# Kernel tuning notes

Hardware: AMD Instinct MI355X
Metric: run time of the kernel (lower is better)

The kernel has to match this reference:

```python
import jax, jax.numpy as jnp
import numpy as np

N = 100000
E = 3200000
IN_DIM = 3
HID = 256
OUT_DIM = 3


def setup_inputs() -> dict:
    key = jax.random.key(0)
    ks = jax.random.split(key, 12)
    x = jax.random.normal(ks[0], (N, IN_DIM), dtype=jnp.float32)
    edge_index = jax.random.randint(ks[1], (2, E), 0, N, dtype=jnp.int64)
    def lin(k, fi, fo):
        k1, k2 = jax.random.split(k)
        bound = 1.0 / np.sqrt(fi)
        W = jax.random.uniform(k1, (fi, fo), jnp.float32, -bound, bound)
        b = jax.random.uniform(k2, (fo,), jnp.float32, -bound, bound)
        return W, b
    W0, b0 = lin(ks[2], IN_DIM, HID)
    W1, b1 = lin(ks[3], HID, HID)
    W2, b2 = lin(ks[4], HID, HID)
    W3, b3 = lin(ks[5], HID, OUT_DIM)
    Wr, br = lin(ks[6], IN_DIM, OUT_DIM)
    return {"x": x, "edge_index": edge_index,
            "W0": W0, "b0": b0, "W1": W1, "b1": b1,
            "W2": W2, "b2": b2, "W3": W3, "b3": b3,
            "Wr": Wr, "br": br}


def reference(x, edge_index, W0, b0, W1, b1, W2, b2, W3, b3, Wr, br):
    n = x.shape[0]
    # add self loops, mirroring build_adjacency_matrix
    loops = jnp.arange(n, dtype=edge_index.dtype)
    row = jnp.concatenate([edge_index[0], loops])
    col = jnp.concatenate([edge_index[1], loops])
    # degree of row endpoints, D^{-1/2}[row] * D^{-1/2}[col] edge weights
    deg = jax.ops.segment_sum(jnp.ones_like(row, dtype=x.dtype), row, num_segments=n)
    dinv = jnp.where(deg > 0, jax.lax.rsqrt(deg), 0.0)
    norm = dinv[row] * dinv[col]  # [E+N]

    def propagate(h):
        # A_hat @ h : gather source features, scale, scatter-add to rows
        return jax.ops.segment_sum(norm[:, None] * h[col], row, num_segments=n)

    h = jax.nn.relu(propagate(x) @ W0 + b0)
    h = jax.nn.relu(propagate(h) @ W1 + b1)
    h = jax.nn.relu(propagate(h) @ W2 + b2)
    h = propagate(h) @ W3 + b3  # last layer: no relu
    return h + (x @ Wr + br)
```

## Files before the change

kernel.cpp:

```cpp
#include <hip/hip_runtime.h>
#include <stdint.h>

typedef unsigned short u16;
typedef unsigned int u32;
typedef __attribute__((ext_vector_type(8))) short short8;
typedef __attribute__((ext_vector_type(4))) float f32x4;

#define CAP 6144
#define TILE 4096

__device__ __forceinline__ float b2f_bits(u32 bits){ union{u32 u; float f;} v; v.u=bits; return v.f; }
__device__ __forceinline__ float bf_lo(u32 w){ return b2f_bits(w<<16); }
__device__ __forceinline__ float bf_hi(u32 w){ return b2f_bits(w & 0xffff0000u); }
__device__ __forceinline__ u16 f2bf(float f){
  union{float f; u32 u;} v; v.f=f;
  return (u16)((v.u + 0x7fffu + ((v.u>>16)&1u))>>16);
}

__global__ void zero_k(int* __restrict__ p, int n){
  int i = blockIdx.x*256 + threadIdx.x;
  if(i<n) p[i]=0;
}

__global__ void detect_k(const long long* __restrict__ ei, int* __restrict__ flag, int n, int E){
  __shared__ int sh[256];
  int t = threadIdx.x;
  int lim = E/2 < 2048 ? E/2 : 2048;
  int bad = 0;
  for(int e=t; e<lim; e+=256){
    unsigned long long v = (unsigned long long)ei[e];
    if(v >= (unsigned long long)n) bad = 1;
  }
  sh[t]=bad; __syncthreads();
  for(int off=128; off>0; off>>=1){ if(t<off) sh[t] |= sh[t+off]; __syncthreads(); }
  if(t==0) *flag = sh[0];
}

__device__ __forceinline__ int edge_at(const void* eiv, int is32, long long idx){
  return is32 ? ((const int*)eiv)[idx] : (int)((const long long*)eiv)[idx];
}
__device__ __forceinline__ int clampi(int v, int lo, int hi){
  return v < lo ? lo : (v > hi ? hi : v);
}

__global__ __launch_bounds__(256) void binA_k(const void* __restrict__ eiv, const int* __restrict__ flag,
                        int* __restrict__ gcur, u32* __restrict__ gbuf, int E, int n, int nbuck){
  __shared__ int hist[1024];
  __shared__ int base[1024];
  __shared__ int cur[1024];
  __shared__ int wsum[256];
  __shared__ u32 stage[TILE];
  int t = threadIdx.x;
  long long e0 = (long long)blockIdx.x * TILE;
  int cnt = (int)((long long)E - e0 < TILE ? (long long)E - e0 : TILE);
  int is32 = *flag;
  for(int i=t; i<nbuck; i+=256){ hist[i]=0; cur[i]=0; }
  __syncthreads();
  int eb[16]; u32 ep[16]; int ec=0;
  #pragma unroll
  for(int k=0;k<16;k++){
    int i = t + k*256;
    if(i<cnt){
      long long e = e0 + i;
      int r = clampi(edge_at(eiv,is32,e),0,n-1);
      int c = clampi(edge_at(eiv,is32,(long long)E+e),0,n-1);
      eb[ec] = r>>7;
      ep[ec] = ((u32)(r&127)<<17) | (u32)c;
      atomicAdd(&hist[eb[ec]],1);
      ec++;
    }
  }
  __syncthreads();
  int l[4]; int tot=0;
  #pragma unroll
  for(int j=0;j<4;j++){ int idx=t*4+j; l[j]=(idx<nbuck)?hist[idx]:0; tot+=l[j]; }
  wsum[t]=tot; __syncthreads();
  for(int off=1;off<256;off<<=1){
    int x = (t>=off)?wsum[t-off]:0;
    __syncthreads();
    wsum[t]+=x;
    __syncthreads();
  }
  int excl = wsum[t]-tot;
  #pragma unroll
  for(int j=0;j<4;j++){ int idx=t*4+j; if(idx<nbuck) base[idx]=excl; excl+=l[j]; }
  __syncthreads();
  for(int k=0;k<ec;k++){
    int b = eb[k];
    int slot = base[b] + atomicAdd(&cur[b],1);
    stage[slot] = ep[k];
  }
  __syncthreads();
  for(int b=t; b<nbuck; b+=256){
    int c = hist[b];
    if(c>0){
      int g = atomicAdd(&gcur[b], c);
      if(g > CAP) g = CAP;
      if(g + c > CAP) c = CAP - g;
      int src = base[b];
      u32* dst = gbuf + (size_t)b*CAP + g;
      for(int k=0;k<c;k++) dst[k] = stage[src+k];
    }
  }
}

__global__ __launch_bounds__(256) void degB_k(const int* __restrict__ gcnt, const u32* __restrict__ gbuf,
                        int* __restrict__ deg, int n, int nbuck){
  __shared__ int h[128];
  int b = blockIdx.x, t = threadIdx.x;
  if(t<128) h[t]=0;
  __syncthreads();
  int c = gcnt[b]; if(c>CAP) c=CAP;
  const u32* p = gbuf + (size_t)b*CAP;
  for(int i=t;i<c;i+=256) atomicAdd(&h[p[i]>>17],1);
  __syncthreads();
  int row = b*128 + t;
  if(t<128 && row<n) deg[row]=h[t];
}

__global__ void dinv_k(const int* __restrict__ deg, float* __restrict__ dinv, int n){
  int i = blockIdx.x*256 + threadIdx.x;
  if(i<n) dinv[i] = rsqrtf((float)(deg[i] + 1));
}

__global__ __launch_bounds__(256) void scan1_k(const int* __restrict__ deg, int* __restrict__ bsum, int m){
  __shared__ int sh[256];
  int b = blockIdx.x, t = threadIdx.x;
  int base = b*4096 + t*16;
  int s = 0;
  #pragma unroll
  for(int j=0;j<16;j++){ int i = base+j; if(i<m) s += deg[i]; }
  sh[t]=s; __syncthreads();
  for(int off=128; off>0; off>>=1){ if(t<off) sh[t] += sh[t+off]; __syncthreads(); }
  if(t==0) bsum[b] = sh[0];
}

__global__ __launch_bounds__(256) void scan2_k(int* __restrict__ bsum, int nb){
  __shared__ int sh[256];
  int t = threadIdx.x;
  int v = (t<nb) ? bsum[t] : 0;
  sh[t]=v; __syncthreads();
  for(int off=1; off<256; off<<=1){
    int x = (t>=off) ? sh[t-off] : 0;
    __syncthreads();
    sh[t] += x;
    __syncthreads();
  }
  if(t<nb) bsum[t] = sh[t] - v;
}

__global__ __launch_bounds__(256) void scan3_k(const int* __restrict__ deg, const int* __restrict__ bscan,
                        int* __restrict__ rs, int m){
  __shared__ int sh[256];
  int b = blockIdx.x, t = threadIdx.x;
  int base = b*4096 + t*16;
  int v[16]; int s = 0;
  #pragma unroll
  for(int j=0;j<16;j++){ v[j] = (base+j<m) ? deg[base+j] : 0; s += v[j]; }
  sh[t]=s; __syncthreads();
  for(int off=1; off<256; off<<=1){
    int x = (t>=off) ? sh[t-off] : 0;
    __syncthreads();
    sh[t] += x;
    __syncthreads();
  }
  int excl = sh[t] - s + bscan[b];
  #pragma unroll
  for(int j=0;j<16;j++){
    if(base+j<m){ rs[base+j]=excl; excl += v[j]; }
  }
}

__global__ __launch_bounds__(256) void csrB_k(const int* __restrict__ gcnt, const u32* __restrict__ gbuf,
                        const int* __restrict__ rs, const int* __restrict__ deg,
                        int* __restrict__ csr, int n, int nbuck){
  __shared__ int sc[128];
  __shared__ int lst[128];
  __shared__ int lcur[128];
  __shared__ int colstage[CAP];
  int b = blockIdx.x, t = threadIdx.x;
  int row0 = b*128;
  int dv = 0;
  if(t<128){ int row=row0+t; dv=(row<n)?deg[row]:0; sc[t]=dv; lcur[t]=0; }
  __syncthreads();
  for(int off=1;off<128;off<<=1){
    int x = (t>=off && t<128) ? sc[t-off] : 0;
    __syncthreads();
    if(t<128) sc[t]+=x;
    __syncthreads();
  }
  if(t<128) lst[t]=sc[t]-dv;
  __syncthreads();
  int c = gcnt[b]; if(c>CAP) c=CAP;
  const u32* p = gbuf + (size_t)b*CAP;
  for(int i=t;i<c;i+=256){
    u32 pr = p[i];
    int rl = pr>>17;
    int slot = lst[rl] + atomicAdd(&lcur[rl],1);
    if(slot < CAP) colstage[slot] = (int)(pr & 0x1FFFFu);
  }
  __syncthreads();
  int tot = sc[127]; if(tot>c) tot=c;
  int gbase = rs[row0];
  for(int i=t;i<tot;i+=256) csr[gbase+i] = colstage[i];
}

__global__ void pack_k(const float* __restrict__ W, u16* __restrict__ out){
  int idx = blockIdx.x*256 + threadIdx.x;
  int j  = idx & 7;
  int l  = (idx>>3) & 63;
  int ct = (idx>>9) & 15;
  int kk = idx>>13;
  int k  = kk*32 + (l>>4)*8 + j;
  int nn = ct*16 + (l&15);
  out[idx] = f2bf(W[k*256 + nn]);
}

__global__ void prop3_k(const float* __restrict__ x, const int* __restrict__ csr,
                        const int* __restrict__ rs, const int* __restrict__ deg,
                        const float* __restrict__ dinv, float* __restrict__ p0, int n){
  int i = blockIdx.x*256 + threadIdx.x;
  if(i>=n) return;
  float a0=0.f, a1=0.f, a2=0.f;
  int s = rs[i], e = s + deg[i];
  for(int t=s; t<e; t++){
    int c = csr[t];
    float w = dinv[c];
    a0 += w*x[c*3+0]; a1 += w*x[c*3+1]; a2 += w*x[c*3+2];
  }
  float di = dinv[i];
  a0 += di*x[i*3+0]; a1 += di*x[i*3+1]; a2 += di*x[i*3+2];
  p0[i*3+0]=di*a0; p0[i*3+1]=di*a1; p0[i*3+2]=di*a2;
}

__global__ __launch_bounds__(256) void prop256_k(const u16* __restrict__ hin, u16* __restrict__ pout,
                          const int* __restrict__ csr, const int* __restrict__ rs,
                          const int* __restrict__ deg, const float* __restrict__ dinv, int n){
  int row = (blockIdx.x*256 + threadIdx.x) >> 6;
  if(row>=n) return;
  row = __builtin_amdgcn_readfirstlane(row);
  int lane = threadIdx.x & 63;
  int co = lane*4;
  const u16* hb = hin + co;
  uint2 sv = *(const uint2*)(hb + (size_t)row*256);
  float a0=bf_lo(sv.x), a1=bf_hi(sv.x), a2=bf_lo(sv.y), a3=bf_hi(sv.y);
  int s = __builtin_amdgcn_readfirstlane(rs[row]);
  int d = __builtin_amdgcn_readfirstlane(deg[row]);
  for(int base=0; base<d; base+=16){
    int cc[16]; u32 mk[16];
    #pragma unroll
    for(int j=0;j<16;j++){
      int ok = (base+j) < d;
      cc[j] = csr[ok ? (s+base+j) : s];
      mk[j] = ok ? 0xffffffffu : 0u;
    }
    uint2 v[16];
    #pragma unroll
    for(int j=0;j<16;j++) v[j] = *(const uint2*)(hb + (size_t)cc[j]*256);
    #pragma unroll
    for(int j=0;j<16;j++){
      u32 xw = v[j].x & mk[j], yw = v[j].y & mk[j];
      a0 += bf_lo(xw); a1 += bf_hi(xw); a2 += bf_lo(yw); a3 += bf_hi(yw);
    }
  }
  float sc = dinv[row];
  uint2 o;
  o.x = (u32)f2bf(a0*sc) | ((u32)f2bf(a1*sc)<<16);
  o.y = (u32)f2bf(a2*sc) | ((u32)f2bf(a3*sc)<<16);
  *(uint2*)(pout + (size_t)row*256 + co) = o;
}

__global__ __launch_bounds__(256) void gemm0_k(const float* __restrict__ p0, const float* __restrict__ W0,
                        const float* __restrict__ b0, const float* __restrict__ dinv,
                        u16* __restrict__ h1, int n){
  int i = blockIdx.x;
  int j = threadIdx.x;
  float v = p0[i*3+0]*W0[j] + p0[i*3+1]*W0[256+j] + p0[i*3+2]*W0[512+j] + b0[j];
  v = fmaxf(v, 0.f) * dinv[i];
  h1[(size_t)i*256 + j] = f2bf(v);
}

__global__ __launch_bounds__(256) void gemm256_k(const u16* __restrict__ A, const u16* __restrict__ Bp,
                          const float* __restrict__ bias, const float* __restrict__ dinv,
                          u16* __restrict__ Out, int M){
  int wave = threadIdx.x>>6, lane = threadIdx.x&63;
  int rowbase = blockIdx.x*64 + wave*16;
  f32x4 acc[16];
  #pragma unroll
  for(int t=0;t<16;t++){ acc[t][0]=0.f; acc[t][1]=0.f; acc[t][2]=0.f; acc[t][3]=0.f; }
  const u16* Ap = A + (size_t)(rowbase + (lane&15))*256 + ((lane>>4)*8);
  const u16* Bl = Bp + (size_t)lane*8;
  #pragma unroll
  for(int kk=0; kk<8; kk++){
    short8 af = *(const short8*)(Ap + kk*32);
    const u16* bb = Bl + (size_t)kk*8192;
    #pragma unroll
    for(int t=0;t<16;t++){
      short8 bf = *(const short8*)(bb + t*512);
      acc[t] = __builtin_amdgcn_mfma_f32_16x16x32_bf16(af, bf, acc[t], 0, 0, 0);
    }
  }
  int r0 = rowbase + (lane>>4)*4;
  float dv[4]; bool ok[4];
  #pragma unroll
  for(int r=0;r<4;r++){ ok[r] = (r0+r) < M; dv[r] = ok[r] ? dinv[r0+r] : 0.f; }
  #pragma unroll
  for(int t=0;t<16;t++){
    int col = t*16 + (lane&15);
    float bc = bias[col];
    #pragma unroll
    for(int r=0;r<4;r++){
      if(ok[r]){
        float v = fmaxf(acc[t][r] + bc, 0.f) * dv[r];
        Out[(size_t)(r0+r)*256 + col] = f2bf(v);
      }
    }
  }
}

__global__ __launch_bounds__(256) void gemm3_k(const u16* __restrict__ h3, const float* __restrict__ W3,
                        float* __restrict__ qh, int n){
  __shared__ float w3s[768];
  for(int i=threadIdx.x; i<768; i+=256) w3s[i] = W3[i];
  __syncthreads();
  int i = blockIdx.x*256 + threadIdx.x;
  if(i>=n) return;
  float a0=0.f, a1=0.f, a2=0.f;
  const uint4* hp = (const uint4*)(h3 + (size_t)i*256);
  for(int kk=0; kk<32; kk++){
    uint4 v = hp[kk];
    float f[8] = {bf_lo(v.x),bf_hi(v.x),bf_lo(v.y),bf_hi(v.y),
                  bf_lo(v.z),bf_hi(v.z),bf_lo(v.w),bf_hi(v.w)};
    int k0 = kk*8;
    #pragma unroll
    for(int j=0;j<8;j++){
      a0 += f[j]*w3s[(k0+j)*3+0];
      a1 += f[j]*w3s[(k0+j)*3+1];
      a2 += f[j]*w3s[(k0+j)*3+2];
    }
  }
  qh[i*3+0]=a0; qh[i*3+1]=a1; qh[i*3+2]=a2;
}

__global__ void final_k(const float* __restrict__ qh, const float* __restrict__ x,
                        const int* __restrict__ csr, const int* __restrict__ rs,
                        const int* __restrict__ deg, const float* __restrict__ dinv,
                        const float* __restrict__ b3, const float* __restrict__ Wr,
                        const float* __restrict__ br, float* __restrict__ out, int n){
  int i = blockIdx.x*256 + threadIdx.x;
  if(i>=n) return;
  float a0=0.f, a1=0.f, a2=0.f;
  int s = rs[i], e = s + deg[i];
  for(int t=s; t<e; t++){
    int c = csr[t];
    a0 += qh[c*3+0]; a1 += qh[c*3+1]; a2 += qh[c*3+2];
  }
  float di = dinv[i];
  a0 = di*(a0 + qh[i*3+0]);
  a1 = di*(a1 + qh[i*3+1]);
  a2 = di*(a2 + qh[i*3+2]);
  float x0=x[i*3+0], x1=x[i*3+1], x2=x[i*3+2];
  out[i*3+0] = a0 + b3[0] + x0*Wr[0] + x1*Wr[3] + x2*Wr[6] + br[0];
  out[i*3+1] = a1 + b3[1] + x0*Wr[1] + x1*Wr[4] + x2*Wr[7] + br[1];
  out[i*3+2] = a2 + b3[2] + x0*Wr[2] + x1*Wr[5] + x2*Wr[8] + br[2];
}

extern "C" void kernel_launch(void* const* d_in, const int* in_sizes, int n_in,
                              void* d_out, int out_size, void* d_ws, size_t ws_size,
                              hipStream_t stream) {
  const float* x  = (const float*)d_in[0];
  const void*  ei = d_in[1];
  const float* W0 = (const float*)d_in[2];
  const float* b0 = (const float*)d_in[3];
  const float* W1 = (const float*)d_in[4];
  const float* b1 = (const float*)d_in[5];
  const float* W2 = (const float*)d_in[6];
  const float* b2 = (const float*)d_in[7];
  const float* W3 = (const float*)d_in[8];
  const float* b3 = (const float*)d_in[9];
  const float* Wr = (const float*)d_in[10];
  const float* br = (const float*)d_in[11];
  float* out = (float*)d_out;

  int n = in_sizes[0]/3;
  int E = in_sizes[1]/2;
  int nbuck = (n+127)>>7;
  int Mpad = ((n+63)/64)*64;
  int nbscan = (n+4095)/4096;

  char* p = (char*)d_ws;
  auto alloc = [&](size_t bytes)->char*{ char* r=p; p += (bytes+255)&~(size_t)255; return r; };
  int*   gcur  = (int*)  alloc((size_t)nbuck*4);
  int*   deg   = (int*)  alloc((size_t)n*4);
  float* dinv  = (float*)alloc((size_t)n*4);
  int*   rs    = (int*)  alloc((size_t)n*4);
  int*   bsum  = (int*)  alloc(256*4);
  int*   flag  = (int*)  alloc(256);
  int*   csr   = (int*)  alloc((size_t)E*4);
  u16*   hA    = (u16*)  alloc((size_t)Mpad*512);
  u16*   hB    = (u16*)  alloc((size_t)Mpad*512);
  float* p0    = (float*)alloc((size_t)n*12);
  float* qh    = (float*)alloc((size_t)n*12);
  u16*   W1p   = (u16*)  alloc(65536*2);
  u16*   W2p   = (u16*)  alloc(65536*2);
  u32*   gbuf  = (u32*)hA;

  int gn  = (n+255)/256;
  int gA  = (E+TILE-1)/TILE;
  int gp  = (n*64+255)/256;

  zero_k  <<<(nbuck+255)/256, 256, 0, stream>>>(gcur, nbuck);
  detect_k<<<1, 256, 0, stream>>>((const long long*)ei, flag, n, E);
  binA_k  <<<gA, 256, 0, stream>>>(ei, flag, gcur, gbuf, E, n, nbuck);
  degB_k  <<<nbuck, 256, 0, stream>>>(gcur, gbuf, deg, n, nbuck);
  dinv_k  <<<gn, 256, 0, stream>>>(deg, dinv, n);
  scan1_k <<<nbscan, 256, 0, stream>>>(deg, bsum, n);
  scan2_k <<<1, 256, 0, stream>>>(bsum, nbscan);
  scan3_k <<<nbscan, 256, 0, stream>>>(deg, bsum, rs, n);
  csrB_k  <<<nbuck, 256, 0, stream>>>(gcur, gbuf, rs, deg, csr, n, nbuck);

  pack_k  <<<256, 256, 0, stream>>>(W1, W1p);
  pack_k  <<<256, 256, 0, stream>>>(W2, W2p);

  prop3_k <<<gn, 256, 0, stream>>>(x, csr, rs, deg, dinv, p0, n);
  gemm0_k <<<n, 256, 0, stream>>>(p0, W0, b0, dinv, hA, n);

  prop256_k<<<gp, 256, 0, stream>>>(hA, hB, csr, rs, deg, dinv, n);
  gemm256_k<<<Mpad/64, 256, 0, stream>>>(hB, W1p, b1, dinv, hA, n);

  prop256_k<<<gp, 256, 0, stream>>>(hA, hB, csr, rs, deg, dinv, n);
  gemm256_k<<<Mpad/64, 256, 0, stream>>>(hB, W2p, b2, dinv, hA, n);

  gemm3_k <<<gn, 256, 0, stream>>>(hA, W3, qh, n);
  final_k <<<gn, 256, 0, stream>>>(qh, x, csr, rs, deg, dinv, b3, Wr, br, out, n);
}
```

Before: 907.9 us.

## Fuse CSR build kernels, merge weight packing, process two rows per wave in propagation

Folds the gcur zeroing into the detect kernel. Replaces the degree, dinv, three-pass scan and CSR kernels with a single bucket-level scan plus one fused CSR kernel that computes degree, dinv and row starts from the bucket histogram. The two weight-pack launches are merged into one. The 256-wide propagation now splits each wave into two halves, each handling one row with 16-byte loads (8 bf16 per lane) and 8-edge batches, to cut launch count and widen memory transactions. In exchange, a half-wave idles when its row has fewer neighbours than its partner row.

```diff
diff --git a/kernel.cpp b/kernel.cpp
--- a/kernel.cpp
+++ b/kernel.cpp
@@ -17,14 +17,12 @@
   return (u16)((v.u + 0x7fffu + ((v.u>>16)&1u))>>16);
 }
 
-__global__ void zero_k(int* __restrict__ p, int n){
-  int i = blockIdx.x*256 + threadIdx.x;
-  if(i<n) p[i]=0;
-}
-
-__global__ void detect_k(const long long* __restrict__ ei, int* __restrict__ flag, int n, int E){
+
+__global__ void detect_k(const long long* __restrict__ ei, int* __restrict__ flag,
+                         int* __restrict__ gcur, int n, int E, int nbuck){
   __shared__ int sh[256];
   int t = threadIdx.x;
+  for(int i=t; i<nbuck; i+=256) gcur[i]=0;
   int lim = E/2 < 2048 ? E/2 : 2048;
   int bad = 0;
   for(int e=t; e<lim; e+=256){
@@ -104,109 +102,77 @@
   }
 }
 
-__global__ __launch_bounds__(256) void degB_k(const int* __restrict__ gcnt, const u32* __restrict__ gbuf,
-                        int* __restrict__ deg, int n, int nbuck){
-  __shared__ int h[128];
+__global__ __launch_bounds__(256) void scanG_k(const int* __restrict__ gcnt, int* __restrict__ gstart, int nbuck){
+  __shared__ int sh[256];
+  int t = threadIdx.x;
+  int v[4]; int s=0;
+  #pragma unroll
+  for(int j=0;j<4;j++){
+    int idx=t*4+j;
+    int c = (idx<nbuck)?gcnt[idx]:0;
+    if(c>CAP) c=CAP;
+    v[j]=c; s+=c;
+  }
+  sh[t]=s; __syncthreads();
+  for(int off=1;off<256;off<<=1){
+    int x=(t>=off)?sh[t-off]:0;
+    __syncthreads();
+    sh[t]+=x;
+    __syncthreads();
+  }
+  int excl = sh[t]-s;
+  #pragma unroll
+  for(int j=0;j<4;j++){ int idx=t*4+j; if(idx<nbuck) gstart[idx]=excl; excl+=v[j]; }
+}
+
+__global__ __launch_bounds__(256) void csrB_k(const int* __restrict__ gcnt, const int* __restrict__ gstart,
+                        const u32* __restrict__ gbuf, int* __restrict__ deg, float* __restrict__ dinv,
+                        int* __restrict__ rs, int* __restrict__ csr, int n, int nbuck){
+  __shared__ int h[128], lst[128], lcur[128], sc[128];
+  __shared__ int colstage[CAP];
   int b = blockIdx.x, t = threadIdx.x;
-  if(t<128) h[t]=0;
+  if(t<128){ h[t]=0; lcur[t]=0; }
   __syncthreads();
   int c = gcnt[b]; if(c>CAP) c=CAP;
   const u32* p = gbuf + (size_t)b*CAP;
   for(int i=t;i<c;i+=256) atomicAdd(&h[p[i]>>17],1);
   __syncthreads();
-  int row = b*128 + t;
-  if(t<128 && row<n) deg[row]=h[t];
-}
-
-__global__ void dinv_k(const int* __restrict__ deg, float* __restrict__ dinv, int n){
-  int i = blockIdx.x*256 + threadIdx.x;
-  if(i<n) dinv[i] = rsqrtf((float)(deg[i] + 1));
-}
-
-__global__ __launch_bounds__(256) void scan1_k(const int* __restrict__ deg, int* __restrict__ bsum, int m){
-  __shared__ int sh[256];
-  int b = blockIdx.x, t = threadIdx.x;
-  int base = b*4096 + t*16;
-  int s = 0;
-  #pragma unroll
-  for(int j=0;j<16;j++){ int i = base+j; if(i<m) s += deg[i]; }
-  sh[t]=s; __syncthreads();
-  for(int off=128; off>0; off>>=1){ if(t<off) sh[t] += sh[t+off]; __syncthreads(); }
-  if(t==0) bsum[b] = sh[0];
-}
-
-__global__ __launch_bounds__(256) void scan2_k(int* __restrict__ bsum, int nb){
-  __shared__ int sh[256];
-  int t = threadIdx.x;
-  int v = (t<nb) ? bsum[t] : 0;
-  sh[t]=v; __syncthreads();
-  for(int off=1; off<256; off<<=1){
-    int x = (t>=off) ? sh[t-off] : 0;
-    __syncthreads();
-    sh[t] += x;
-    __syncthreads();
-  }
-  if(t<nb) bsum[t] = sh[t] - v;
-}
-
-__global__ __launch_bounds__(256) void scan3_k(const int* __restrict__ deg, const int* __restrict__ bscan,
-                        int* __restrict__ rs, int m){
-  __shared__ int sh[256];
-  int b = blockIdx.x, t = threadIdx.x;
-  int base = b*4096 + t*16;
-  int v[16]; int s = 0;
-  #pragma unroll
-  for(int j=0;j<16;j++){ v[j] = (base+j<m) ? deg[base+j] : 0; s += v[j]; }
-  sh[t]=s; __syncthreads();
-  for(int off=1; off<256; off<<=1){
-    int x = (t>=off) ? sh[t-off] : 0;
-    __syncthreads();
-    sh[t] += x;
-    __syncthreads();
-  }
-  int excl = sh[t] - s + bscan[b];
-  #pragma unroll
-  for(int j=0;j<16;j++){
-    if(base+j<m){ rs[base+j]=excl; excl += v[j]; }
-  }
-}
-
-__global__ __launch_bounds__(256) void csrB_k(const int* __restrict__ gcnt, const u32* __restrict__ gbuf,
-                        const int* __restrict__ rs, const int* __restrict__ deg,
-                        int* __restrict__ csr, int n, int nbuck){
-  __shared__ int sc[128];
-  __shared__ int lst[128];
-  __shared__ int lcur[128];
-  __shared__ int colstage[CAP];
-  int b = blockIdx.x, t = threadIdx.x;
-  int row0 = b*128;
-  int dv = 0;
-  if(t<128){ int row=row0+t; dv=(row<n)?deg[row]:0; sc[t]=dv; lcur[t]=0; }
+  int dv=0;
+  if(t<128){ dv=h[t]; sc[t]=dv; }
   __syncthreads();
   for(int off=1;off<128;off<<=1){
-    int x = (t>=off && t<128) ? sc[t-off] : 0;
+    int x=(t>=off&&t<128)?sc[t-off]:0;
     __syncthreads();
     if(t<128) sc[t]+=x;
     __syncthreads();
   }
-  if(t<128) lst[t]=sc[t]-dv;
-  __syncthreads();
-  int c = gcnt[b]; if(c>CAP) c=CAP;
-  const u32* p = gbuf + (size_t)b*CAP;
+  int g0 = gstart[b];
+  if(t<128){
+    lst[t]=sc[t]-dv;
+    int row=b*128+t;
+    if(row<n){
+      deg[row]=dv;
+      dinv[row]=rsqrtf((float)(dv+1));
+      rs[row]=g0+lst[t];
+    }
+  }
+  __syncthreads();
   for(int i=t;i<c;i+=256){
-    u32 pr = p[i];
-    int rl = pr>>17;
-    int slot = lst[rl] + atomicAdd(&lcur[rl],1);
-    if(slot < CAP) colstage[slot] = (int)(pr & 0x1FFFFu);
-  }
-  __syncthreads();
-  int tot = sc[127]; if(tot>c) tot=c;
-  int gbase = rs[row0];
-  for(int i=t;i<tot;i+=256) csr[gbase+i] = colstage[i];
-}
-
-__global__ void pack_k(const float* __restrict__ W, u16* __restrict__ out){
-  int idx = blockIdx.x*256 + threadIdx.x;
+    u32 pr=p[i];
+    int rl=pr>>17;
+    int slot=lst[rl]+atomicAdd(&lcur[rl],1);
+    if(slot<CAP) colstage[slot]=(int)(pr&0x1FFFFu);
+  }
+  __syncthreads();
+  for(int i=t;i<c;i+=256) csr[g0+i]=colstage[i];
+}
+
+__global__ void pack2_k(const float* __restrict__ W1, const float* __restrict__ W2,
+                        u16* __restrict__ o1, u16* __restrict__ o2){
+  int bid = blockIdx.x;
+  const float* W = (bid<256)? W1 : W2;
+  u16* out = (bid<256)? o1 : o2;
+  int idx = (bid&255)*256 + threadIdx.x;
   int j  = idx & 7;
   int l  = (idx>>3) & 63;
   int ct = (idx>>9) & 15;
@@ -233,41 +199,53 @@
   p0[i*3+0]=di*a0; p0[i*3+1]=di*a1; p0[i*3+2]=di*a2;
 }
 
-__global__ __launch_bounds__(256) void prop256_k(const u16* __restrict__ hin, u16* __restrict__ pout,
+__global__ __launch_bounds__(256) void prop2x_k(const u16* __restrict__ hin, u16* __restrict__ pout,
                           const int* __restrict__ csr, const int* __restrict__ rs,
                           const int* __restrict__ deg, const float* __restrict__ dinv, int n){
-  int row = (blockIdx.x*256 + threadIdx.x) >> 6;
-  if(row>=n) return;
-  row = __builtin_amdgcn_readfirstlane(row);
+  int pair = (blockIdx.x*256 + threadIdx.x) >> 6;
+  int r0 = pair*2;
+  if(r0>=n) return;
   int lane = threadIdx.x & 63;
-  int co = lane*4;
-  const u16* hb = hin + co;
-  uint2 sv = *(const uint2*)(hb + (size_t)row*256);
-  float a0=bf_lo(sv.x), a1=bf_hi(sv.x), a2=bf_lo(sv.y), a3=bf_hi(sv.y);
-  int s = __builtin_amdgcn_readfirstlane(rs[row]);
-  int d = __builtin_amdgcn_readfirstlane(deg[row]);
-  for(int base=0; base<d; base+=16){
-    int cc[16]; u32 mk[16];
-    #pragma unroll
-    for(int j=0;j<16;j++){
+  int half = lane>>5;
+  int li = lane & 31;
+  int row = r0 + half;
+  int rok = row < n;
+  int rowc = rok ? row : r0;
+  const u16* hb = hin + li*8;
+  uint4 sv = *(const uint4*)(hb + (size_t)rowc*256);
+  float a[8];
+  a[0]=bf_lo(sv.x); a[1]=bf_hi(sv.x); a[2]=bf_lo(sv.y); a[3]=bf_hi(sv.y);
+  a[4]=bf_lo(sv.z); a[5]=bf_hi(sv.z); a[6]=bf_lo(sv.w); a[7]=bf_hi(sv.w);
+  int s = rs[rowc];
+  int d = rok ? deg[rowc] : 0;
+  int dmax = max(d, __shfl_xor(d, 32));
+  for(int base=0; base<dmax; base+=8){
+    int cc[8]; u32 mk[8];
+    #pragma unroll
+    for(int j=0;j<8;j++){
       int ok = (base+j) < d;
       cc[j] = csr[ok ? (s+base+j) : s];
       mk[j] = ok ? 0xffffffffu : 0u;
     }
-    uint2 v[16];
-    #pragma unroll
-    for(int j=0;j<16;j++) v[j] = *(const uint2*)(hb + (size_t)cc[j]*256);
-    #pragma unroll
-    for(int j=0;j<16;j++){
-      u32 xw = v[j].x & mk[j], yw = v[j].y & mk[j];
-      a0 += bf_lo(xw); a1 += bf_hi(xw); a2 += bf_lo(yw); a3 += bf_hi(yw);
-    }
-  }
-  float sc = dinv[row];
-  uint2 o;
-  o.x = (u32)f2bf(a0*sc) | ((u32)f2bf(a1*sc)<<16);
-  o.y = (u32)f2bf(a2*sc) | ((u32)f2bf(a3*sc)<<16);
-  *(uint2*)(pout + (size_t)row*256 + co) = o;
+    uint4 v[8];
+    #pragma unroll
+    for(int j=0;j<8;j++) v[j] = *(const uint4*)(hb + (size_t)cc[j]*256);
+    #pragma unroll
+    for(int j=0;j<8;j++){
+      u32 w0=v[j].x&mk[j], w1=v[j].y&mk[j], w2=v[j].z&mk[j], w3=v[j].w&mk[j];
+      a[0]+=bf_lo(w0); a[1]+=bf_hi(w0); a[2]+=bf_lo(w1); a[3]+=bf_hi(w1);
+      a[4]+=bf_lo(w2); a[5]+=bf_hi(w2); a[6]+=bf_lo(w3); a[7]+=bf_hi(w3);
+    }
+  }
+  if(rok){
+    float sc = dinv[row];
+    uint4 o;
+    o.x=(u32)f2bf(a[0]*sc)|((u32)f2bf(a[1]*sc)<<16);
+    o.y=(u32)f2bf(a[2]*sc)|((u32)f2bf(a[3]*sc)<<16);
+    o.z=(u32)f2bf(a[4]*sc)|((u32)f2bf(a[5]*sc)<<16);
+    o.w=(u32)f2bf(a[6]*sc)|((u32)f2bf(a[7]*sc)<<16);
+    *(uint4*)(pout + (size_t)row*256 + li*8) = o;
+  }
 }
 
 __global__ __launch_bounds__(256) void gemm0_k(const float* __restrict__ p0, const float* __restrict__ W0,
@@ -386,15 +364,14 @@
   int E = in_sizes[1]/2;
   int nbuck = (n+127)>>7;
   int Mpad = ((n+63)/64)*64;
-  int nbscan = (n+4095)/4096;
 
   char* p = (char*)d_ws;
   auto alloc = [&](size_t bytes)->char*{ char* r=p; p += (bytes+255)&~(size_t)255; return r; };
   int*   gcur  = (int*)  alloc((size_t)nbuck*4);
+  int*   gstart= (int*)  alloc((size_t)nbuck*4);
   int*   deg   = (int*)  alloc((size_t)n*4);
   float* dinv  = (float*)alloc((size_t)n*4);
   int*   rs    = (int*)  alloc((size_t)n*4);
-  int*   bsum  = (int*)  alloc(256*4);
   int*   flag  = (int*)  alloc(256);
   int*   csr   = (int*)  alloc((size_t)E*4);
   u16*   hA    = (u16*)  alloc((size_t)Mpad*512);
@@ -407,28 +384,22 @@
 
   int gn  = (n+255)/256;
   int gA  = (E+TILE-1)/TILE;
-  int gp  = (n*64+255)/256;
-
-  zero_k  <<<(nbuck+255)/256, 256, 0, stream>>>(gcur, nbuck);
-  detect_k<<<1, 256, 0, stream>>>((const long long*)ei, flag, n, E);
+  int gp2 = (((n+1)/2)*64 + 255)/256;
+
+  detect_k<<<1, 256, 0, stream>>>((const long long*)ei, flag, gcur, n, E, nbuck);
   binA_k  <<<gA, 256, 0, stream>>>(ei, flag, gcur, gbuf, E, n, nbuck);
-  degB_k  <<<nbuck, 256, 0, stream>>>(gcur, gbuf, deg, n, nbuck);
-  dinv_k  <<<gn, 256, 0, stream>>>(deg, dinv, n);
-  scan1_k <<<nbscan, 256, 0, stream>>>(deg, bsum, n);
-  scan2_k <<<1, 256, 0, stream>>>(bsum, nbscan);
-  scan3_k <<<nbscan, 256, 0, stream>>>(deg, bsum, rs, n);
-  csrB_k  <<<nbuck, 256, 0, stream>>>(gcur, gbuf, rs, deg, csr, n, nbuck);
-
-  pack_k  <<<256, 256, 0, stream>>>(W1, W1p);
-  pack_k  <<<256, 256, 0, stream>>>(W2, W2p);
+  scanG_k <<<1, 256, 0, stream>>>(gcur, gstart, nbuck);
+  csrB_k  <<<nbuck, 256, 0, stream>>>(gcur, gstart, gbuf, deg, dinv, rs, csr, n, nbuck);
+
+  pack2_k <<<512, 256, 0, stream>>>(W1, W2, W1p, W2p);
 
   prop3_k <<<gn, 256, 0, stream>>>(x, csr, rs, deg, dinv, p0, n);
   gemm0_k <<<n, 256, 0, stream>>>(p0, W0, b0, dinv, hA, n);
 
-  prop256_k<<<gp, 256, 0, stream>>>(hA, hB, csr, rs, deg, dinv, n);
+  prop2x_k<<<gp2, 256, 0, stream>>>(hA, hB, csr, rs, deg, dinv, n);
   gemm256_k<<<Mpad/64, 256, 0, stream>>>(hB, W1p, b1, dinv, hA, n);
 
-  prop256_k<<<gp, 256, 0, stream>>>(hA, hB, csr, rs, deg, dinv, n);
+  prop2x_k<<<gp2, 256, 0, stream>>>(hA, hB, csr, rs, deg, dinv, n);
   gemm256_k<<<Mpad/64, 256, 0, stream>>>(hB, W2p, b2, dinv, hA, n);
 
   gemm3_k <<<gn, 256, 0, stream>>>(hA, W3, qh, n);
```

Result: no change. 906.6 us (-0.1%).
